# Optimization experiments

Hardware: AMD Instinct MI355X
Metric: run time of the kernel (lower is better)

## Reference

```python
import jax, jax.numpy as jnp
import numpy as np

N_NODES = 50000
N_EDGES = 400000
N_GRAPHS = 256
NUM_TYPES = 200
EMB = 64
HID = 128
HEADS = 4
GDIM = 256  # graph_embed_dim
NUM_CLASSES = 20
EPS = 1e-5
NEG_SLOPE = 0.2


def _gat_conv(h, src, dst, W, a_src, a_dst, bias, heads, out_c, concat):
    """PyG GATConv (with self-loops already appended to src/dst)."""
    n = h.shape[0]
    x = (h @ W.T).reshape(n, heads, out_c)                       # [N,H,C]
    al_s = jnp.einsum('nhc,hc->nh', x, a_src)                    # [N,H]
    al_d = jnp.einsum('nhc,hc->nh', x, a_dst)
    e = jax.nn.leaky_relu(al_s[src] + al_d[dst], NEG_SLOPE)      # [E',H]
    # segment softmax over destination node
    e_max = jax.ops.segment_max(e, dst, num_segments=n)
    e_exp = jnp.exp(e - e_max[dst])
    denom = jax.ops.segment_sum(e_exp, dst, num_segments=n)
    alpha = e_exp / denom[dst]                                   # [E',H]
    out = jax.ops.segment_sum(alpha[:, :, None] * x[src], dst, num_segments=n)  # [N,H,C]
    out = out.reshape(n, heads * out_c) if concat else out.mean(axis=1)
    return out + bias


def _batchnorm(h, gamma, beta):
    # training-mode BatchNorm1d over node dim (biased variance, as torch)
    m = h.mean(axis=0)
    v = jnp.mean((h - m) ** 2, axis=0)
    return (h - m) * jax.lax.rsqrt(v + EPS) * gamma + beta


def setup_inputs() -> dict:
    key = jax.random.key(0)
    ks = jax.random.split(key, 32)
    s = 0.1
    inp = {
        'x': jax.random.randint(ks[0], (N_NODES,), 0, NUM_TYPES),
        'edge_index': jax.random.randint(ks[1], (2, N_EDGES), 0, N_NODES),
        'depth': jax.random.uniform(ks[2], (N_NODES,), jnp.float32),
        'batch': jnp.sort(jax.random.randint(ks[3], (N_NODES,), 0, N_GRAPHS)),
        'emb_table': jax.random.normal(ks[4], (NUM_TYPES, EMB), jnp.float32) * s,
        'depth_w': jax.random.normal(ks[5], (EMB, 1), jnp.float32) * s,
        'depth_b': jnp.zeros((EMB,), jnp.float32),
        'W0': jax.random.normal(ks[6], (HEADS * HID, EMB), jnp.float32) * s,
        'as0': jax.random.normal(ks[7], (HEADS, HID), jnp.float32) * s,
        'ad0': jax.random.normal(ks[8], (HEADS, HID), jnp.float32) * s,
        'b0': jnp.zeros((HEADS * HID,), jnp.float32),
        'g0': jnp.ones((HEADS * HID,), jnp.float32),
        'be0': jnp.zeros((HEADS * HID,), jnp.float32),
        'W1': jax.random.normal(ks[9], (HEADS * HID, HEADS * HID), jnp.float32) * s,
        'as1': jax.random.normal(ks[10], (HEADS, HID), jnp.float32) * s,
        'ad1': jax.random.normal(ks[11], (HEADS, HID), jnp.float32) * s,
        'b1': jnp.zeros((HEADS * HID,), jnp.float32),
        'g1': jnp.ones((HEADS * HID,), jnp.float32),
        'be1': jnp.zeros((HEADS * HID,), jnp.float32),
        # layer 2: 512 -> 128, 1 head, no concat
        'W2': jax.random.normal(ks[12], (GDIM // 2, HEADS * HID), jnp.float32) * s,
        'as2': jax.random.normal(ks[13], (1, GDIM // 2), jnp.float32) * s,
        'ad2': jax.random.normal(ks[14], (1, GDIM // 2), jnp.float32) * s,
        'b2': jnp.zeros((GDIM // 2,), jnp.float32),
        'g2': jnp.ones((GDIM // 2,), jnp.float32),
        'be2': jnp.zeros((GDIM // 2,), jnp.float32),
        # classifier: 256 -> 256 -> 20
        'cw1': jax.random.normal(ks[15], (GDIM, 2 * (GDIM // 2)), jnp.float32) * s,
        'cb1': jnp.zeros((GDIM,), jnp.float32),
        'cw2': jax.random.normal(ks[16], (NUM_CLASSES, GDIM), jnp.float32) * s,
        'cb2': jnp.zeros((NUM_CLASSES,), jnp.float32),
    }
    return inp


def reference(x, edge_index, depth, batch, emb_table, depth_w, depth_b,
              W0, as0, ad0, b0, g0, be0,
              W1, as1, ad1, b1, g1, be1,
              W2, as2, ad2, b2, g2, be2,
              cw1, cb1, cw2, cb2):
    n = x.shape[0]
    # node features: type embedding + depth projection
    h = emb_table[x] + (depth[:, None] @ depth_w.T + depth_b)    # [N,64]
    # add self-loops once (PyG GATConv default add_self_loops=True)
    loop = jnp.arange(n)
    src = jnp.concatenate([edge_index[0], loop])
    dst = jnp.concatenate([edge_index[1], loop])
    layers = [
        (W0, as0, ad0, b0, g0, be0, HEADS, HID, True),
        (W1, as1, ad1, b1, g1, be1, HEADS, HID, True),
        (W2, as2, ad2, b2, g2, be2, 1, GDIM // 2, False),
    ]
    for (W, a_s, a_d, b, g, be, heads, out_c, concat) in layers:
        h = _gat_conv(h, src, dst, W, a_s, a_d, b, heads, out_c, concat)
        h = _batchnorm(h, g, be)
        h = jax.nn.elu(h)
        # dropout: eval mode -> identity
    # global mean / max pooling per graph
    ones = jnp.ones((n,), h.dtype)
    counts = jax.ops.segment_sum(ones, batch, num_segments=N_GRAPHS)
    h_mean = jax.ops.segment_sum(h, batch, num_segments=N_GRAPHS) / jnp.maximum(counts, 1.0)[:, None]
    h_max = jax.ops.segment_max(h, batch, num_segments=N_GRAPHS)
    emb = jnp.concatenate([h_mean, h_max], axis=-1)              # [G,256]
    # classifier (dropout off in eval)
    hidden = jax.nn.relu(emb @ cw1.T + cb1)
    return hidden @ cw2.T + cb2                                  # [G,20]
```

## Files before the change

kernel.cpp:

```cpp
#include <hip/hip_runtime.h>

#define N_NODES 50000
#define N_PAD 50048
#define NBY 391
#define N_EDGES 400000
#define EP (N_EDGES + N_NODES)
#define N_GRAPHS 256
#define EMB 64
#define HID 128
#define HEADS 4
#define GDIM 256
#define NUM_CLASSES 20
#define EPS_BN 1e-5f
#define NEG_SLOPE 0.2f
#define NB_AGG 2048

typedef __attribute__((ext_vector_type(4))) float f32x4;
typedef _Float16 h8 __attribute__((ext_vector_type(8)));
typedef _Float16 h4 __attribute__((ext_vector_type(4)));
typedef _Float16 h2 __attribute__((ext_vector_type(2)));

#define GLD(g, l)                                                              \
    __builtin_amdgcn_global_load_lds(                                          \
        (const __attribute__((address_space(1))) void*)(g),                    \
        (__attribute__((address_space(3))) void*)(l), 16, 0, 0)

__global__ void k_node_init(const int* __restrict__ x, const float* __restrict__ depth,
                            const float* __restrict__ emb_table, const float* __restrict__ dw,
                            const float* __restrict__ db, float* __restrict__ h) {
    int i = blockIdx.x * blockDim.x + threadIdx.x;
    if (i >= N_NODES * EMB) return;
    int n = i >> 6, c = i & 63;
    h[i] = emb_table[x[n] * EMB + c] + depth[n] * dw[c] + db[c];
}

__global__ void k_deg(const int* __restrict__ ei, int* __restrict__ deg) {
    int e = blockIdx.x * blockDim.x + threadIdx.x;
    if (e >= EP) return;
    int dst = (e < N_EDGES) ? ei[N_EDGES + e] : (e - N_EDGES);
    atomicAdd(&deg[dst], 1);
}

__global__ void k_scanA(const int* __restrict__ deg, int* __restrict__ incl, int* __restrict__ bsums) {
    __shared__ int sh[1024];
    int t = threadIdx.x;
    int i = blockIdx.x * 1024 + t;
    int v = (i < N_NODES) ? deg[i] : 0;
    int xv = v;
    sh[t] = xv;
    __syncthreads();
    for (int off = 1; off < 1024; off <<= 1) {
        int y = (t >= off) ? sh[t - off] : 0;
        __syncthreads();
        xv += y;
        sh[t] = xv;
        __syncthreads();
    }
    if (i < N_NODES) incl[i] = xv;
    if (t == 1023) bsums[blockIdx.x] = xv;
}

__global__ void k_scanC(const int* __restrict__ incl, const int* __restrict__ deg,
                        const int* __restrict__ bsums, int* __restrict__ offs) {
    int i = blockIdx.x * blockDim.x + threadIdx.x;
    int b = i >> 10;
    int add = 0;
    for (int k = 0; k < b; k++) add += bsums[k];
    if (i < N_NODES) offs[i] = incl[i] - deg[i] + add;
    if (i == 0) offs[N_NODES] = EP;
}

__global__ void k_scatter(const int* __restrict__ ei, const int* __restrict__ offs,
                          int* __restrict__ cnt, int* __restrict__ csr) {
    int e = blockIdx.x * blockDim.x + threadIdx.x;
    if (e >= EP) return;
    int src, dst;
    if (e < N_EDGES) { src = ei[e]; dst = ei[N_EDGES + e]; }
    else { src = e - N_EDGES; dst = src; }
    int pos = atomicAdd(&cnt[dst], 1);
    csr[offs[dst] + pos] = src;
}

__device__ __forceinline__ void cvt1(const float* __restrict__ in, _Float16* __restrict__ o, int i) {
    int f = i * 4;
    float4 v = *(const float4*)(in + f);
    h4 r;
    r[0] = (_Float16)v.x; r[1] = (_Float16)v.y; r[2] = (_Float16)v.z; r[3] = (_Float16)v.w;
    *(h4*)(o + f) = r;
}

__global__ __launch_bounds__(256) void k_setup(const float* __restrict__ W0, const float* __restrict__ as0,
                                               const float* __restrict__ ad0, const float* __restrict__ W1,
                                               const float* __restrict__ W2,
                                               _Float16* __restrict__ W0f, _Float16* __restrict__ W1f,
                                               _Float16* __restrict__ W2f,
                                               float* __restrict__ wtil,
                                               float* __restrict__ bn0, float* __restrict__ bn1,
                                               float* __restrict__ bn2) {
    int b = blockIdx.x, t = threadIdx.x;
    if (b < 256) {
        cvt1(W1, W1f, b * 256 + t);
    } else if (b < 288) {
        cvt1(W0, W0f, (b - 256) * 256 + t);
    } else if (b < 352) {
        cvt1(W2, W2f, (b - 288) * 256 + t);
    } else if (b == 352) {
        int h = t >> 6, k = t & 63;
        float ss = 0.f, sd = 0.f;
        for (int c = 0; c < 128; c++) {
            float w = W0[(size_t)(h * 128 + c) * 64 + k];
            ss += w * as0[h * 128 + c];
            sd += w * ad0[h * 128 + c];
        }
        wtil[t] = ss;
        wtil[256 + t] = sd;
    } else {
        for (int i = t; i < 1024; i += 256) { bn0[i] = 0.f; bn1[i] = 0.f; bn2[i] = 0.f; }
    }
}

__global__ __launch_bounds__(256) void k_bnelu(_Float16* __restrict__ a,
                                               const float* __restrict__ sums,
                                               const float* __restrict__ gamma,
                                               const float* __restrict__ beta) {
    const int lane = threadIdx.x & 63;
    const int wid = threadIdx.x >> 6;
    const int c0 = lane * 8;
    const float invN = 1.f / (float)N_NODES;
    float sc[8], sh[8];
#pragma unroll
    for (int k = 0; k < 8; k += 4) {
        float4 s4 = *(const float4*)(sums + c0 + k);
        float4 q4 = *(const float4*)(sums + 512 + c0 + k);
        float4 g4 = *(const float4*)(gamma + c0 + k);
        float4 b4 = *(const float4*)(beta + c0 + k);
        float m, v;
        m = s4.x * invN; v = q4.x * invN - m * m;
        sc[k + 0] = g4.x * __frsqrt_rn(v + EPS_BN); sh[k + 0] = b4.x - m * sc[k + 0];
        m = s4.y * invN; v = q4.y * invN - m * m;
        sc[k + 1] = g4.y * __frsqrt_rn(v + EPS_BN); sh[k + 1] = b4.y - m * sc[k + 1];
        m = s4.z * invN; v = q4.z * invN - m * m;
        sc[k + 2] = g4.z * __frsqrt_rn(v + EPS_BN); sh[k + 2] = b4.z - m * sc[k + 2];
        m = s4.w * invN; v = q4.w * invN - m * m;
        sc[k + 3] = g4.w * __frsqrt_rn(v + EPS_BN); sh[k + 3] = b4.w - m * sc[k + 3];
    }
    const int stride = gridDim.x * 4;
    for (int n = blockIdx.x * 4 + wid; n < N_NODES; n += stride) {
        _Float16* p = a + (size_t)n * 512 + c0;
        h8 v = *(h8*)p;
        h8 o;
#pragma unroll
        for (int k = 0; k < 8; k++) {
            float x = (float)v[k] * sc[k] + sh[k];
            x = x > 0.f ? x : expm1f(x);
            o[k] = (_Float16)x;
        }
        *(h8*)p = o;
    }
}

__global__ __launch_bounds__(256) void k_al0(const float* __restrict__ h0,
                                             const float* __restrict__ wtil,
                                             float* __restrict__ als, float* __restrict__ ald) {
    int wid = threadIdx.x >> 6, lane = threadIdx.x & 63;
    int n = blockIdx.x * 4 + wid;
    if (n >= N_NODES) return;
    float v = h0[(size_t)n * 64 + lane];
#pragma unroll
    for (int h = 0; h < 4; h++) {
        float ps = v * wtil[h * 64 + lane];
        float pd = v * wtil[256 + h * 64 + lane];
        for (int off = 32; off; off >>= 1) {
            ps += __shfl_xor(ps, off);
            pd += __shfl_xor(pd, off);
        }
        if (lane == 0) { als[n * 4 + h] = ps; ald[n * 4 + h] = pd; }
    }
}

__global__ __launch_bounds__(256) void k_agg0(const float* __restrict__ h0,
                                              const float* __restrict__ als,
                                              const float* __restrict__ ald_g,
                                              const int* __restrict__ offs,
                                              const int* __restrict__ csr,
                                              _Float16* __restrict__ outh) {
    const int lane = threadIdx.x & 63;
    const int wwid = threadIdx.x >> 6;
    const int q = lane >> 4, l = lane & 15;
    const int gw = blockIdx.x * 4 + wwid;
    const int stride = gridDim.x * 16;
    for (int n = gw * 4 + q; n < N_NODES; n += stride) {
        int s0 = offs[n], s1 = offs[n + 1];
        float aldl = (l < 4) ? ald_g[n * 4 + l] : 0.f;
        float acc[4][4] = {};
        float den[4] = {};
        int e = s0;
        for (; e + 2 <= s1; e += 2) {
            int srcA = csr[e], srcB = csr[e + 1];
            float wA = 0.f, wB = 0.f;
            if (l < 4) {
                float a1 = als[srcA * 4 + l] + aldl;
                a1 = a1 > 0.f ? a1 : NEG_SLOPE * a1;
                wA = expf(a1);
                float a2 = als[srcB * 4 + l] + aldl;
                a2 = a2 > 0.f ? a2 : NEG_SLOPE * a2;
                wB = expf(a2);
            }
            float4 vA = *(const float4*)(h0 + (size_t)srcA * 64 + l * 4);
            float4 vB = *(const float4*)(h0 + (size_t)srcB * 64 + l * 4);
#pragma unroll
            for (int h = 0; h < 4; h++) {
                float whA = __shfl(wA, q * 16 + h);
                float whB = __shfl(wB, q * 16 + h);
                den[h] += whA + whB;
                acc[h][0] += whA * vA.x + whB * vB.x;
                acc[h][1] += whA * vA.y + whB * vB.y;
                acc[h][2] += whA * vA.z + whB * vB.z;
                acc[h][3] += whA * vA.w + whB * vB.w;
            }
        }
        for (; e < s1; e++) {
            int src = csr[e];
            float w = 0.f;
            if (l < 4) {
                float a1 = als[src * 4 + l] + aldl;
                a1 = a1 > 0.f ? a1 : NEG_SLOPE * a1;
                w = expf(a1);
            }
            float4 v = *(const float4*)(h0 + (size_t)src * 64 + l * 4);
#pragma unroll
            for (int h = 0; h < 4; h++) {
                float wh = __shfl(w, q * 16 + h);
                den[h] += wh;
                acc[h][0] += wh * v.x;
                acc[h][1] += wh * v.y;
                acc[h][2] += wh * v.z;
                acc[h][3] += wh * v.w;
            }
        }
#pragma unroll
        for (int h = 0; h < 4; h++) {
            float id = 1.f / den[h];
            h4 hv;
            hv[0] = (_Float16)(acc[h][0] * id);
            hv[1] = (_Float16)(acc[h][1] * id);
            hv[2] = (_Float16)(acc[h][2] * id);
            hv[3] = (_Float16)(acc[h][3] * id);
            *(h4*)(outh + (size_t)n * 256 + h * 64 + l * 4) = hv;
        }
    }
}

__global__ __launch_bounds__(256) void k_gemm0h(const _Float16* __restrict__ A,
                                                const _Float16* __restrict__ W,
                                                const float* __restrict__ bias,
                                                _Float16* __restrict__ outA,
                                                float* __restrict__ bnacc) {
    __shared__ h8 sA[2][512], sW[2][512];
    const int nbx = gridDim.x;
    const int d = blockIdx.y * nbx + blockIdx.x;
    const int by = (d / (8 * nbx)) * 8 + (d & 7);
    const int bx = (d >> 3) % nbx;
    if (by >= NBY) return;
    const int hd = bx;
    const int t = threadIdx.x;
    const int lane = t & 63;
    const int wid = t >> 6;
    const int wm = wid >> 1, wn = wid & 1;
    const int r0 = by * 128;
    const int l15 = lane & 15, quad = lane >> 4;
    f32x4 acc[4][4] = {};
    auto stage = [&](int buf, int kb) {
#pragma unroll
        for (int r = 0; r < 2; r++) {
            int c = r * 256 + t;
            int row = c >> 2, q = c & 3;
            size_t gA = ((size_t)(r0 + row) * 256 + hd * 64 + kb) * 2 + q * 16;
            size_t gW = ((size_t)(hd * 128 + row) * 64 + kb) * 2 + q * 16;
            GLD((const char*)A + gA, (char*)&sA[buf][0] + c * 16);
            GLD((const char*)W + gW, (char*)&sW[buf][0] + c * 16);
        }
    };
    stage(0, 0);
    __syncthreads();
#pragma unroll
    for (int ki = 0; ki < 2; ki++) {
        int cur = ki & 1;
        if (ki + 1 < 2) stage(cur ^ 1, (ki + 1) * 32);
        h8 a[4], w[4];
#pragma unroll
        for (int i = 0; i < 4; i++) {
            a[i] = sA[cur][(wm * 64 + i * 16 + l15) * 4 + quad];
            w[i] = sW[cur][(wn * 64 + i * 16 + l15) * 4 + quad];
        }
#pragma unroll
        for (int i = 0; i < 4; i++)
#pragma unroll
            for (int j = 0; j < 4; j++)
                acc[i][j] = __builtin_amdgcn_mfma_f32_16x16x32_f16(a[i], w[j], acc[i][j], 0, 0, 0);
        __syncthreads();
    }
    float colsum[4] = {}, colsq[4] = {};
#pragma unroll
    for (int i = 0; i < 4; i++) {
        int gr = r0 + wm * 64 + i * 16 + quad * 4;
#pragma unroll
        for (int j = 0; j < 4; j++) {
            int gc = hd * 128 + wn * 64 + j * 16 + l15;
            float bv = bias[gc];
#pragma unroll
            for (int rg = 0; rg < 4; rg++) {
                int rr = gr + rg;
                if (rr < N_NODES) {
                    float o = acc[i][j][rg] + bv;
                    outA[(size_t)rr * 512 + gc] = (_Float16)o;
                    colsum[j] += o;
                    colsq[j] += o * o;
                }
            }
        }
    }
#pragma unroll
    for (int j = 0; j < 4; j++) {
        colsum[j] += __shfl_xor(colsum[j], 16);
        colsum[j] += __shfl_xor(colsum[j], 32);
        colsq[j] += __shfl_xor(colsq[j], 16);
        colsq[j] += __shfl_xor(colsq[j], 32);
    }
    float* sS = (float*)&sA[0][0];
    float* sQ = (float*)&sW[0][0];
    __syncthreads();
    if (quad == 0) {
#pragma unroll
        for (int j = 0; j < 4; j++) {
            int c = wn * 64 + j * 16 + l15;
            sS[c * 2 + wm] = colsum[j];
            sQ[c * 2 + wm] = colsq[j];
        }
    }
    __syncthreads();
    if (t < 128) {
        atomicAdd(bnacc + hd * 128 + t, sS[t * 2] + sS[t * 2 + 1]);
        atomicAdd(bnacc + 512 + hd * 128 + t, sQ[t * 2] + sQ[t * 2 + 1]);
    }
}

__global__ __launch_bounds__(256) void k_gemm_mfma(const _Float16* __restrict__ A,
                                                   const _Float16* __restrict__ W,
                                                   const float* __restrict__ a_src,
                                                   const float* __restrict__ a_dst,
                                                   float* __restrict__ als_g,
                                                   float* __restrict__ ald_g,
                                                   _Float16* __restrict__ out,
                                                   int K, int M, int heads) {
    __shared__ h8 sA[2][512], sW[2][512];
    const int nbx = gridDim.x;
    const int d = blockIdx.y * nbx + blockIdx.x;
    const int by = (d / (8 * nbx)) * 8 + (d & 7);
    const int bx = (d >> 3) % nbx;
    if (by >= NBY) return;
    const int t = threadIdx.x;
    const int lane = t & 63;
    const int wid = t >> 6;
    const int wm = wid >> 1, wn = wid & 1;
    const int r0 = by * 128, c0 = bx * 128;
    const int l15 = lane & 15, quad = lane >> 4;
    f32x4 acc[4][4] = {};
    auto stage = [&](int buf, int kb) {
#pragma unroll
        for (int r = 0; r < 2; r++) {
            int c = r * 256 + t;
            int row = c >> 2, q = c & 3;
            size_t gA = ((size_t)(r0 + row) * K + kb) * 2 + q * 16;
            size_t gW = ((size_t)(c0 + row) * K + kb) * 2 + q * 16;
            GLD((const char*)A + gA, (char*)&sA[buf][0] + c * 16);
            GLD((const char*)W + gW, (char*)&sW[buf][0] + c * 16);
        }
    };
    stage(0, 0);
    __syncthreads();
    const int nkb = K >> 5;
    for (int ki = 0; ki < nkb; ki++) {
        int cur = ki & 1;
        if (ki + 1 < nkb) stage(cur ^ 1, (ki + 1) * 32);
        h8 a[4], w[4];
#pragma unroll
        for (int i = 0; i < 4; i++) {
            a[i] = sA[cur][(wm * 64 + i * 16 + l15) * 4 + quad];
            w[i] = sW[cur][(wn * 64 + i * 16 + l15) * 4 + quad];
        }
#pragma unroll
        for (int i = 0; i < 4; i++)
#pragma unroll
            for (int j = 0; j < 4; j++)
                acc[i][j] = __builtin_amdgcn_mfma_f32_16x16x32_f16(a[i], w[j], acc[i][j], 0, 0, 0);
        __syncthreads();
    }
#pragma unroll
    for (int i = 0; i < 4; i++) {
        int gr = r0 + wm * 64 + i * 16 + quad * 4;
#pragma unroll
        for (int j = 0; j < 4; j++) {
            int gc = c0 + wn * 64 + j * 16 + l15;
#pragma unroll
            for (int rg = 0; rg < 4; rg++) {
                int rr = gr + rg;
                if (rr < N_NODES) out[(size_t)rr * M + gc] = (_Float16)acc[i][j][rg];
            }
        }
    }
    const int hd = bx;
    float ps[4][4] = {}, pd[4][4] = {};
#pragma unroll
    for (int j = 0; j < 4; j++) {
        int ch = wn * 64 + j * 16 + l15;
        float av = a_src[hd * 128 + ch];
        float dv = a_dst[hd * 128 + ch];
#pragma unroll
        for (int i = 0; i < 4; i++)
#pragma unroll
            for (int rg = 0; rg < 4; rg++) {
                ps[i][rg] += acc[i][j][rg] * av;
                pd[i][rg] += acc[i][j][rg] * dv;
            }
    }
#pragma unroll
    for (int m = 1; m < 16; m <<= 1)
#pragma unroll
        for (int i = 0; i < 4; i++)
#pragma unroll
            for (int rg = 0; rg < 4; rg++) {
                ps[i][rg] += __shfl_xor(ps[i][rg], m);
                pd[i][rg] += __shfl_xor(pd[i][rg], m);
            }
    float* sS = (float*)&sA[0][0];
    float* sD = (float*)&sW[0][0];
    if (l15 == 0) {
#pragma unroll
        for (int i = 0; i < 4; i++)
#pragma unroll
            for (int rg = 0; rg < 4; rg++) {
                int ri = wm * 64 + i * 16 + quad * 4 + rg;
                sS[ri * 2 + wn] = ps[i][rg];
                sD[ri * 2 + wn] = pd[i][rg];
            }
    }
    __syncthreads();
    if (t < 128) {
        int row = r0 + t;
        if (row < N_NODES) {
            als_g[row * heads + hd] = sS[t * 2] + sS[t * 2 + 1];
            ald_g[row * heads + hd] = sD[t * 2] + sD[t * 2 + 1];
        }
    }
}

__global__ __launch_bounds__(256) void k_agg512(const _Float16* __restrict__ xf,
                                                const float* __restrict__ als,
                                                const float* __restrict__ ald_g,
                                                const int* __restrict__ offs,
                                                const int* __restrict__ csr,
                                                const float* __restrict__ bias,
                                                _Float16* __restrict__ out16,
                                                float* __restrict__ bnacc) {
    __shared__ float pool[4][1024];
    const int wid = threadIdx.x >> 6, lane = threadIdx.x & 63;
    int* s_src = (int*)&pool[wid][0];
    float* s_w = &pool[wid][64];
    const int gw = blockIdx.x * 4 + wid;
    const int nw = gridDim.x * 4;
    const int hh = lane >> 4;
    const int c0 = lane * 8;
    float bias8[8];
#pragma unroll
    for (int k = 0; k < 8; k++) bias8[k] = bias[c0 + k];
    float bns[8] = {}, bnq[8] = {};
    for (int n = gw; n < N_NODES; n += nw) {
        int s0 = offs[n], s1 = offs[n + 1];
        float4 aldv = *(const float4*)(ald_g + n * 4);
        float a[8] = {};
        float den = 0.f;
        for (int base = s0; base < s1; base += 64) {
            int j = base + lane;
            int srcj = 0;
            float4 alv = make_float4(0.f, 0.f, 0.f, 0.f);
            if (j < s1) {
                srcj = csr[j];
                alv = *(const float4*)(als + srcj * 4);
            }
            float e0 = alv.x + aldv.x; e0 = e0 > 0.f ? e0 : NEG_SLOPE * e0;
            float e1 = alv.y + aldv.y; e1 = e1 > 0.f ? e1 : NEG_SLOPE * e1;
            float e2 = alv.z + aldv.z; e2 = e2 > 0.f ? e2 : NEG_SLOPE * e2;
            float e3 = alv.w + aldv.w; e3 = e3 > 0.f ? e3 : NEG_SLOPE * e3;
            s_src[lane] = srcj;
            s_w[0 * 64 + lane] = expf(e0);
            s_w[1 * 64 + lane] = expf(e1);
            s_w[2 * 64 + lane] = expf(e2);
            s_w[3 * 64 + lane] = expf(e3);
            int cend = min(64, s1 - base);
            int e = 0;
            for (; e + 8 <= cend; e += 8) {
                h8 v[8];
                float w[8];
#pragma unroll
                for (int u = 0; u < 8; u++) {
                    v[u] = *(const h8*)(xf + (size_t)s_src[e + u] * 512 + c0);
                    w[u] = s_w[hh * 64 + e + u];
                }
#pragma unroll
                for (int u = 0; u < 8; u++) {
                    den += w[u];
#pragma unroll
                    for (int k = 0; k < 8; k++) a[k] += w[u] * (float)v[u][k];
                }
            }
            for (; e + 2 <= cend; e += 2) {
                h8 vA = *(const h8*)(xf + (size_t)s_src[e] * 512 + c0);
                h8 vB = *(const h8*)(xf + (size_t)s_src[e + 1] * 512 + c0);
                float wA = s_w[hh * 64 + e], wB = s_w[hh * 64 + e + 1];
                den += wA + wB;
#pragma unroll
                for (int k = 0; k < 8; k++) a[k] += wA * (float)vA[k] + wB * (float)vB[k];
            }
            if (e < cend) {
                h8 v = *(const h8*)(xf + (size_t)s_src[e] * 512 + c0);
                float w = s_w[hh * 64 + e];
                den += w;
#pragma unroll
                for (int k = 0; k < 8; k++) a[k] += w * (float)v[k];
            }
        }
        float id = 1.f / den;
        h8 ov;
#pragma unroll
        for (int k = 0; k < 8; k++) {
            float o = a[k] * id + bias8[k];
            ov[k] = (_Float16)o;
            bns[k] += o;
            bnq[k] += o * o;
        }
        *(h8*)(out16 + (size_t)n * 512 + c0) = ov;
    }
#pragma unroll
    for (int k = 0; k < 8; k++) {
        pool[wid][c0 + k] = bns[k];
        pool[wid][512 + c0 + k] = bnq[k];
    }
    __syncthreads();
    for (int t = threadIdx.x; t < 1024; t += 256)
        atomicAdd(bnacc + t, pool[0][t] + pool[1][t] + pool[2][t] + pool[3][t]);
}

__global__ __launch_bounds__(256) void k_agg128(const _Float16* __restrict__ xf,
                                                const float* __restrict__ als,
                                                const float* __restrict__ ald_g,
                                                const int* __restrict__ offs,
                                                const int* __restrict__ csr,
                                                const float* __restrict__ bias,
                                                float* __restrict__ out_f,
                                                float* __restrict__ bnacc) {
    __shared__ float pool[4][256];
    const int wid = threadIdx.x >> 6, lane = threadIdx.x & 63;
    int* s_src = (int*)&pool[wid][0];
    float* s_w = &pool[wid][64];
    const int gw = blockIdx.x * 4 + wid;
    const int nw = gridDim.x * 4;
    const int c = lane * 2;
    const float2 biasv = *(const float2*)(bias + c);
    float bns0 = 0.f, bns1 = 0.f, bnq0 = 0.f, bnq1 = 0.f;
    for (int n = gw; n < N_NODES; n += nw) {
        int s0 = offs[n], s1 = offs[n + 1];
        float aldv = ald_g[n];
        float ax = 0.f, ay = 0.f, den = 0.f;
        for (int base = s0; base < s1; base += 64) {
            int j = base + lane;
            int srcj = 0;
            float alv = 0.f;
            if (j < s1) { srcj = csr[j]; alv = als[srcj]; }
            float e0 = alv + aldv;
            e0 = e0 > 0.f ? e0 : NEG_SLOPE * e0;
            s_src[lane] = srcj;
            s_w[lane] = expf(e0);
            int cend = min(64, s1 - base);
            int e = 0;
            for (; e + 8 <= cend; e += 8) {
                h2 v[8];
                float w[8];
#pragma unroll
                for (int u = 0; u < 8; u++) {
                    v[u] = *(const h2*)(xf + (size_t)s_src[e + u] * 128 + c);
                    w[u] = s_w[e + u];
                }
#pragma unroll
                for (int u = 0; u < 8; u++) {
                    den += w[u];
                    ax += w[u] * (float)v[u][0];
                    ay += w[u] * (float)v[u][1];
                }
            }
            for (; e < cend; e++) {
                h2 v = *(const h2*)(xf + (size_t)s_src[e] * 128 + c);
                float w = s_w[e];
                den += w;
                ax += w * (float)v[0];
                ay += w * (float)v[1];
            }
        }
        float id = 1.f / den;
        float ox = ax * id + biasv.x;
        float oy = ay * id + biasv.y;
        *(float2*)(out_f + (size_t)n * 128 + c) = make_float2(ox, oy);
        bns0 += ox; bnq0 += ox * ox;
        bns1 += oy; bnq1 += oy * oy;
    }
    pool[wid][c] = bns0; pool[wid][c + 1] = bns1;
    pool[wid][128 + c] = bnq0; pool[wid][128 + c + 1] = bnq1;
    __syncthreads();
    {
        int t = threadIdx.x;
        atomicAdd(bnacc + t, pool[0][t] + pool[1][t] + pool[2][t] + pool[3][t]);
    }
}

__global__ void k_graph_bounds(const int* __restrict__ batch, int* __restrict__ goffs) {
    int n = blockIdx.x * blockDim.x + threadIdx.x;
    if (n >= N_NODES) return;
    int b = batch[n];
    int bp = (n == 0) ? -1 : batch[n - 1];
    for (int g = bp + 1; g <= b; g++) goffs[g] = n;
    if (n == N_NODES - 1) {
        for (int g = b + 1; g <= N_GRAPHS; g++) goffs[g] = N_NODES;
    }
}

__global__ __launch_bounds__(256) void k_poolclassify(const float* __restrict__ C,
                                                      const float* __restrict__ bnsums,
                                                      const float* __restrict__ gamma,
                                                      const float* __restrict__ beta,
                                                      const int* __restrict__ goffs,
                                                      const float* __restrict__ cw1, const float* __restrict__ cb1,
                                                      const float* __restrict__ cw2, const float* __restrict__ cb2,
                                                      float* __restrict__ out) {
    __shared__ float er[256];
    __shared__ float red[256];
    int g = blockIdx.x, t = threadIdx.x;
    int c = t & 127, half = t >> 7;
    const float invN = 1.f / (float)N_NODES;
    float m = bnsums[c] * invN;
    float var = bnsums[128 + c] * invN - m * m;
    float sc = gamma[c] * __frsqrt_rn(var + EPS_BN);
    float sh = beta[c] - m * sc;
    int s = goffs[g], e = goffs[g + 1];
    float sum = 0.f, mx = -INFINITY;
    for (int n = s + half; n < e; n += 2) {
        float x = C[(size_t)n * 128 + c] * sc + sh;
        x = x > 0.f ? x : expm1f(x);
        sum += x;
        mx = fmaxf(mx, x);
    }
    red[t] = sum;
    __syncthreads();
    float sumT = red[c] + red[128 + c];
    __syncthreads();
    red[t] = mx;
    __syncthreads();
    float mxT = fmaxf(red[c], red[128 + c]);
    int cnt = e - s;
    if (half == 0) {
        er[c] = sumT / (float)max(cnt, 1);
        er[128 + c] = mxT;
    }
    __syncthreads();
    float acc = cb1[t];
    for (int k = 0; k < 256; k++) acc += er[k] * cw1[t * 256 + k];
    __syncthreads();
    red[t] = fmaxf(acc, 0.f);
    __syncthreads();
    if (t < NUM_CLASSES) {
        float o = cb2[t];
        for (int k = 0; k < 256; k++) o += red[k] * cw2[t * 256 + k];
        out[g * NUM_CLASSES + t] = o;
    }
}

extern "C" void kernel_launch(void* const* d_in, const int* in_sizes, int n_in,
                              void* d_out, int out_size, void* d_ws, size_t ws_size,
                              hipStream_t stream) {
    (void)in_sizes; (void)n_in; (void)out_size; (void)ws_size;
    const int* x = (const int*)d_in[0];
    const int* ei = (const int*)d_in[1];
    const float* depth = (const float*)d_in[2];
    const int* batch = (const int*)d_in[3];
    const float* emb_table = (const float*)d_in[4];
    const float* depth_w = (const float*)d_in[5];
    const float* depth_b = (const float*)d_in[6];
    const float* W0 = (const float*)d_in[7];
    const float* as0 = (const float*)d_in[8];
    const float* ad0 = (const float*)d_in[9];
    const float* b0 = (const float*)d_in[10];
    const float* g0 = (const float*)d_in[11];
    const float* be0 = (const float*)d_in[12];
    const float* W1 = (const float*)d_in[13];
    const float* as1 = (const float*)d_in[14];
    const float* ad1 = (const float*)d_in[15];
    const float* b1 = (const float*)d_in[16];
    const float* g1 = (const float*)d_in[17];
    const float* be1 = (const float*)d_in[18];
    const float* W2 = (const float*)d_in[19];
    const float* as2 = (const float*)d_in[20];
    const float* ad2 = (const float*)d_in[21];
    const float* b2 = (const float*)d_in[22];
    const float* g2 = (const float*)d_in[23];
    const float* be2 = (const float*)d_in[24];
    const float* cw1 = (const float*)d_in[25];
    const float* cb1 = (const float*)d_in[26];
    const float* cw2 = (const float*)d_in[27];
    const float* cb2 = (const float*)d_in[28];
    float* out = (float*)d_out;

    size_t off = 0;
    char* base = (char*)d_ws;
    auto carve = [&](size_t bytes) -> void* {
        void* p = base + off;
        off += (bytes + 255) & ~(size_t)255;
        return p;
    };
    float* B = (float*)carve((size_t)N_NODES * 512 * 2);
    _Float16* A16 = (_Float16*)carve((size_t)N_PAD * 512 * 2);
    _Float16* W0f = (_Float16*)carve((size_t)512 * 64 * 2);
    _Float16* W1f = (_Float16*)carve((size_t)512 * 512 * 2);
    _Float16* W2f = (_Float16*)carve((size_t)128 * 512 * 2);
    float* als = (float*)carve((size_t)N_NODES * HEADS * 4);
    float* ald = (float*)carve((size_t)N_NODES * HEADS * 4);
    float* bn0 = (float*)carve(1024 * 4);
    float* bn1 = (float*)carve(1024 * 4);
    float* bn2 = (float*)carve(1024 * 4);
    float* wtil = (float*)carve(512 * 4);
    int* deg = (int*)carve((size_t)2 * N_NODES * 4);
    int* cnt = deg + N_NODES;
    int* incl = (int*)carve((size_t)N_NODES * 4);
    int* offs = (int*)carve((size_t)(N_NODES + 1) * 4);
    int* bsums = (int*)carve(64 * 4);
    int* csr = (int*)carve((size_t)EP * 4);
    int* goffs = (int*)carve((size_t)(N_GRAPHS + 1) * 4);

    float* h0 = B;
    _Float16* hth = (_Float16*)((char*)B + (size_t)N_NODES * 64 * 4);
    _Float16* Bh = (_Float16*)B;
    float* C = (float*)A16;

    const int TPB = 256;
    int gbN = (N_NODES + TPB - 1) / TPB;
    int gbE = (EP + TPB - 1) / TPB;
    int nbScan = (N_NODES + 1023) / 1024;
    int gbNode4 = (N_NODES + 3) / 4;
    dim3 g512(4, 392);
    dim3 g128(1, 391);

    hipMemsetAsync(deg, 0, (size_t)2 * N_NODES * 4, stream);
    k_setup<<<354, TPB, 0, stream>>>(W0, as0, ad0, W1, W2, W0f, W1f, W2f, wtil, bn0, bn1, bn2);
    k_deg<<<gbE, TPB, 0, stream>>>(ei, deg);
    k_scanA<<<nbScan, 1024, 0, stream>>>(deg, incl, bsums);
    k_scanC<<<gbN, TPB, 0, stream>>>(incl, deg, bsums, offs);
    k_scatter<<<gbE, TPB, 0, stream>>>(ei, offs, cnt, csr);
    k_graph_bounds<<<gbN, TPB, 0, stream>>>(batch, goffs);

    k_node_init<<<(N_NODES * EMB + TPB - 1) / TPB, TPB, 0, stream>>>(x, depth, emb_table, depth_w, depth_b, h0);
    k_al0<<<gbNode4, TPB, 0, stream>>>(h0, wtil, als, ald);
    k_agg0<<<NB_AGG, TPB, 0, stream>>>(h0, als, ald, offs, csr, hth);
    k_gemm0h<<<g512, TPB, 0, stream>>>(hth, W0f, b0, A16, bn0);
    k_bnelu<<<2048, TPB, 0, stream>>>(A16, bn0, g0, be0);
    k_gemm_mfma<<<g512, TPB, 0, stream>>>(A16, W1f, as1, ad1, als, ald, Bh, 512, 512, HEADS);
    k_agg512<<<NB_AGG, TPB, 0, stream>>>(Bh, als, ald, offs, csr, b1, A16, bn1);
    k_bnelu<<<2048, TPB, 0, stream>>>(A16, bn1, g1, be1);
    k_gemm_mfma<<<g128, TPB, 0, stream>>>(A16, W2f, as2, ad2, als, ald, Bh, 512, 128, 1);
    k_agg128<<<NB_AGG, TPB, 0, stream>>>(Bh, als, ald, offs, csr, b2, C, bn2);
    k_poolclassify<<<N_GRAPHS, TPB, 0, stream>>>(C, bn2, g2, be2, goffs, cw1, cb1, cw2, cb2, out);
}
```

Before: 590.5 us.

## Handle self-loops inline, store initial embeddings in fp16, widen agg512 grid

Result: slower. 614.8 us (+4.1%).

```diff
diff --git a/kernel.cpp b/kernel.cpp
--- a/kernel.cpp
+++ b/kernel.cpp
@@ -4,7 +4,6 @@
 #define N_PAD 50048
 #define NBY 391
 #define N_EDGES 400000
-#define EP (N_EDGES + N_NODES)
 #define N_GRAPHS 256
 #define EMB 64
 #define HID 128
@@ -27,18 +26,17 @@
 
 __global__ void k_node_init(const int* __restrict__ x, const float* __restrict__ depth,
                             const float* __restrict__ emb_table, const float* __restrict__ dw,
-                            const float* __restrict__ db, float* __restrict__ h) {
+                            const float* __restrict__ db, _Float16* __restrict__ h) {
     int i = blockIdx.x * blockDim.x + threadIdx.x;
     if (i >= N_NODES * EMB) return;
     int n = i >> 6, c = i & 63;
-    h[i] = emb_table[x[n] * EMB + c] + depth[n] * dw[c] + db[c];
+    h[i] = (_Float16)(emb_table[x[n] * EMB + c] + depth[n] * dw[c] + db[c]);
 }
 
 __global__ void k_deg(const int* __restrict__ ei, int* __restrict__ deg) {
     int e = blockIdx.x * blockDim.x + threadIdx.x;
-    if (e >= EP) return;
-    int dst = (e < N_EDGES) ? ei[N_EDGES + e] : (e - N_EDGES);
-    atomicAdd(&deg[dst], 1);
+    if (e >= N_EDGES) return;
+    atomicAdd(&deg[ei[N_EDGES + e]], 1);
 }
 
 __global__ void k_scanA(const int* __restrict__ deg, int* __restrict__ incl, int* __restrict__ bsums) {
@@ -67,16 +65,14 @@
     int add = 0;
     for (int k = 0; k < b; k++) add += bsums[k];
     if (i < N_NODES) offs[i] = incl[i] - deg[i] + add;
-    if (i == 0) offs[N_NODES] = EP;
+    if (i == 0) offs[N_NODES] = N_EDGES;
 }
 
 __global__ void k_scatter(const int* __restrict__ ei, const int* __restrict__ offs,
                           int* __restrict__ cnt, int* __restrict__ csr) {
     int e = blockIdx.x * blockDim.x + threadIdx.x;
-    if (e >= EP) return;
-    int src, dst;
-    if (e < N_EDGES) { src = ei[e]; dst = ei[N_EDGES + e]; }
-    else { src = e - N_EDGES; dst = src; }
+    if (e >= N_EDGES) return;
+    int src = ei[e], dst = ei[N_EDGES + e];
     int pos = atomicAdd(&cnt[dst], 1);
     csr[offs[dst] + pos] = src;
 }
@@ -159,13 +155,13 @@
     }
 }
 
-__global__ __launch_bounds__(256) void k_al0(const float* __restrict__ h0,
+__global__ __launch_bounds__(256) void k_al0(const _Float16* __restrict__ h16,
                                              const float* __restrict__ wtil,
                                              float* __restrict__ als, float* __restrict__ ald) {
     int wid = threadIdx.x >> 6, lane = threadIdx.x & 63;
     int n = blockIdx.x * 4 + wid;
     if (n >= N_NODES) return;
-    float v = h0[(size_t)n * 64 + lane];
+    float v = (float)h16[(size_t)n * 64 + lane];
 #pragma unroll
     for (int h = 0; h < 4; h++) {
         float ps = v * wtil[h * 64 + lane];
@@ -178,7 +174,7 @@
     }
 }
 
-__global__ __launch_bounds__(256) void k_agg0(const float* __restrict__ h0,
+__global__ __launch_bounds__(256) void k_agg0(const _Float16* __restrict__ h16,
                                               const float* __restrict__ als,
                                               const float* __restrict__ ald_g,
                                               const int* __restrict__ offs,
@@ -194,6 +190,25 @@
         float aldl = (l < 4) ? ald_g[n * 4 + l] : 0.f;
         float acc[4][4] = {};
         float den[4] = {};
+        {
+            float ws = 0.f;
+            if (l < 4) {
+                float a1 = als[n * 4 + l] + aldl;
+                a1 = a1 > 0.f ? a1 : NEG_SLOPE * a1;
+                ws = expf(a1);
+            }
+            h4 vs = *(const h4*)(h16 + (size_t)n * 64 + l * 4);
+            float v0 = (float)vs[0], v1 = (float)vs[1], v2 = (float)vs[2], v3 = (float)vs[3];
+#pragma unroll
+            for (int h = 0; h < 4; h++) {
+                float wh = __shfl(ws, q * 16 + h);
+                den[h] += wh;
+                acc[h][0] += wh * v0;
+                acc[h][1] += wh * v1;
+                acc[h][2] += wh * v2;
+                acc[h][3] += wh * v3;
+            }
+        }
         int e = s0;
         for (; e + 2 <= s1; e += 2) {
             int srcA = csr[e], srcB = csr[e + 1];
@@ -206,17 +221,19 @@
                 a2 = a2 > 0.f ? a2 : NEG_SLOPE * a2;
                 wB = expf(a2);
             }
-            float4 vA = *(const float4*)(h0 + (size_t)srcA * 64 + l * 4);
-            float4 vB = *(const float4*)(h0 + (size_t)srcB * 64 + l * 4);
+            h4 vA = *(const h4*)(h16 + (size_t)srcA * 64 + l * 4);
+            h4 vB = *(const h4*)(h16 + (size_t)srcB * 64 + l * 4);
+            float vA0 = (float)vA[0], vA1 = (float)vA[1], vA2 = (float)vA[2], vA3 = (float)vA[3];
+            float vB0 = (float)vB[0], vB1 = (float)vB[1], vB2 = (float)vB[2], vB3 = (float)vB[3];
 #pragma unroll
             for (int h = 0; h < 4; h++) {
                 float whA = __shfl(wA, q * 16 + h);
                 float whB = __shfl(wB, q * 16 + h);
                 den[h] += whA + whB;
-                acc[h][0] += whA * vA.x + whB * vB.x;
-                acc[h][1] += whA * vA.y + whB * vB.y;
-                acc[h][2] += whA * vA.z + whB * vB.z;
-                acc[h][3] += whA * vA.w + whB * vB.w;
+                acc[h][0] += whA * vA0 + whB * vB0;
+                acc[h][1] += whA * vA1 + whB * vB1;
+                acc[h][2] += whA * vA2 + whB * vB2;
+                acc[h][3] += whA * vA3 + whB * vB3;
             }
         }
         for (; e < s1; e++) {
@@ -227,15 +244,16 @@
                 a1 = a1 > 0.f ? a1 : NEG_SLOPE * a1;
                 w = expf(a1);
             }
-            float4 v = *(const float4*)(h0 + (size_t)src * 64 + l * 4);
+            h4 v = *(const h4*)(h16 + (size_t)src * 64 + l * 4);
+            float v0 = (float)v[0], v1 = (float)v[1], v2 = (float)v[2], v3 = (float)v[3];
 #pragma unroll
             for (int h = 0; h < 4; h++) {
                 float wh = __shfl(w, q * 16 + h);
                 den[h] += wh;
-                acc[h][0] += wh * v.x;
-                acc[h][1] += wh * v.y;
-                acc[h][2] += wh * v.z;
-                acc[h][3] += wh * v.w;
+                acc[h][0] += wh * v0;
+                acc[h][1] += wh * v1;
+                acc[h][2] += wh * v2;
+                acc[h][3] += wh * v3;
             }
         }
 #pragma unroll
@@ -480,6 +498,15 @@
         float4 aldv = *(const float4*)(ald_g + n * 4);
         float a[8] = {};
         float den = 0.f;
+        {
+            float es = als[n * 4 + hh] + ald_g[n * 4 + hh];
+            es = es > 0.f ? es : NEG_SLOPE * es;
+            float ws = expf(es);
+            h8 vs = *(const h8*)(xf + (size_t)n * 512 + c0);
+            den += ws;
+#pragma unroll
+            for (int k = 0; k < 8; k++) a[k] += ws * (float)vs[k];
+        }
         for (int base = s0; base < s1; base += 64) {
             int j = base + lane;
             int srcj = 0;
@@ -572,6 +599,15 @@
         int s0 = offs[n], s1 = offs[n + 1];
         float aldv = ald_g[n];
         float ax = 0.f, ay = 0.f, den = 0.f;
+        {
+            float es = als[n] + aldv;
+            es = es > 0.f ? es : NEG_SLOPE * es;
+            float ws = expf(es);
+            h2 vs = *(const h2*)(xf + (size_t)n * 128 + c);
+            den += ws;
+            ax += ws * (float)vs[0];
+            ay += ws * (float)vs[1];
+        }
         for (int base = s0; base < s1; base += 64) {
             int j = base + lane;
             int srcj = 0;
@@ -741,17 +777,17 @@
     int* incl = (int*)carve((size_t)N_NODES * 4);
     int* offs = (int*)carve((size_t)(N_NODES + 1) * 4);
     int* bsums = (int*)carve(64 * 4);
-    int* csr = (int*)carve((size_t)EP * 4);
+    int* csr = (int*)carve((size_t)N_EDGES * 4);
     int* goffs = (int*)carve((size_t)(N_GRAPHS + 1) * 4);
 
-    float* h0 = B;
-    _Float16* hth = (_Float16*)((char*)B + (size_t)N_NODES * 64 * 4);
+    _Float16* h16 = (_Float16*)B;
+    _Float16* hth = (_Float16*)((char*)B + (size_t)N_NODES * 64 * 2);
     _Float16* Bh = (_Float16*)B;
     float* C = (float*)A16;
 
     const int TPB = 256;
     int gbN = (N_NODES + TPB - 1) / TPB;
-    int gbE = (EP + TPB - 1) / TPB;
+    int gbE = (N_EDGES + TPB - 1) / TPB;
     int nbScan = (N_NODES + 1023) / 1024;
     int gbNode4 = (N_NODES + 3) / 4;
     dim3 g512(4, 392);
@@ -765,13 +801,13 @@
     k_scatter<<<gbE, TPB, 0, stream>>>(ei, offs, cnt, csr);
     k_graph_bounds<<<gbN, TPB, 0, stream>>>(batch, goffs);
 
-    k_node_init<<<(N_NODES * EMB + TPB - 1) / TPB, TPB, 0, stream>>>(x, depth, emb_table, depth_w, depth_b, h0);
-    k_al0<<<gbNode4, TPB, 0, stream>>>(h0, wtil, als, ald);
-    k_agg0<<<NB_AGG, TPB, 0, stream>>>(h0, als, ald, offs, csr, hth);
+    k_node_init<<<(N_NODES * EMB + TPB - 1) / TPB, TPB, 0, stream>>>(x, depth, emb_table, depth_w, depth_b, h16);
+    k_al0<<<gbNode4, TPB, 0, stream>>>(h16, wtil, als, ald);
+    k_agg0<<<NB_AGG, TPB, 0, stream>>>(h16, als, ald, offs, csr, hth);
     k_gemm0h<<<g512, TPB, 0, stream>>>(hth, W0f, b0, A16, bn0);
     k_bnelu<<<2048, TPB, 0, stream>>>(A16, bn0, g0, be0);
     k_gemm_mfma<<<g512, TPB, 0, stream>>>(A16, W1f, as1, ad1, als, ald, Bh, 512, 512, HEADS);
-    k_agg512<<<NB_AGG, TPB, 0, stream>>>(Bh, als, ald, offs, csr, b1, A16, bn1);
+    k_agg512<<<4096, TPB, 0, stream>>>(Bh, als, ald, offs, csr, b1, A16, bn1);
     k_bnelu<<<2048, TPB, 0, stream>>>(A16, bn1, g1, be1);
     k_gemm_mfma<<<g128, TPB, 0, stream>>>(A16, W2f, as2, ad2, als, ald, Bh, 512, 128, 1);
     k_agg128<<<NB_AGG, TPB, 0, stream>>>(Bh, als, ald, offs, csr, b2, C, bn2);
```
